# Performance work log

Measured on AMD Instinct MI355X. Metric: run time of the kernel, lower is better.

The kernel has to match this reference:

```python
import jax, jax.numpy as jnp
import numpy as np

N = 25000
E = 400000
HIDDEN = 512
NH = 8
DH = HIDDEN // NH


def setup_inputs() -> dict:
    key = jax.random.key(0)
    ks = jax.random.split(key, 10)
    s = 1.0 / np.sqrt(HIDDEN)
    return {
        "h": jax.random.normal(ks[0], (N, HIDDEN), dtype=jnp.float32),
        "Wq": jax.random.normal(ks[1], (HIDDEN, HIDDEN), dtype=jnp.float32) * s,
        "bq": jnp.zeros((HIDDEN,), dtype=jnp.float32),
        "Wk": jax.random.normal(ks[2], (HIDDEN, HIDDEN), dtype=jnp.float32) * s,
        "bk": jnp.zeros((HIDDEN,), dtype=jnp.float32),
        "Wo": jax.random.normal(ks[3], (HIDDEN, HIDDEN), dtype=jnp.float32) * s,
        "bo": jnp.zeros((HIDDEN,), dtype=jnp.float32),
        "rows": jax.random.randint(ks[4], (E,), 0, N, dtype=jnp.int32),
        "cols": jax.random.randint(ks[5], (E,), 0, N, dtype=jnp.int32),
    }


def reference(h, Wq, bq, Wk, bk, Wo, bo, rows, cols):
    # Projections; reshape (N, dh, nh) exactly as the source does.
    q = (h @ Wq + bq).reshape(N, DH, NH)
    k = (h @ Wk + bk).reshape(N, DH, NH)
    v = k  # source bug kept faithfully: v = linear_k(h)

    # SDDMM: per-edge, per-head dot product (no 1/sqrt(dh) scaling in source).
    scores = jnp.einsum("edh,edh->eh", q[rows], k[cols])  # [E, NH]

    # Row-wise (source-node) segment softmax per head.
    m = jax.ops.segment_max(scores, rows, num_segments=N)       # [N, NH]
    ex = jnp.exp(scores - m[rows])                              # [E, NH]
    denom = jax.ops.segment_sum(ex, rows, num_segments=N)      # [N, NH]
    attn = ex / denom[rows]                                     # [E, NH]

    # SpMM: out[i] = sum_{j in nbr(i)} attn[ij] * v[j]
    msgs = attn[:, None, :] * v[cols]                           # [E, DH, NH]
    out = jax.ops.segment_sum(msgs, rows, num_segments=N)      # [N, DH, NH]

    return out.reshape(N, HIDDEN) @ Wo + bo
```

## Files before the change

kernel.cpp:

```cpp
#include <hip/hip_runtime.h>
#include <math.h>

typedef unsigned short u16;
typedef unsigned int u32;
typedef __attribute__((ext_vector_type(8))) _Float16 half8;
typedef __attribute__((ext_vector_type(2))) _Float16 half2v;
typedef __attribute__((ext_vector_type(8))) u16 ushort8;
typedef __attribute__((ext_vector_type(4))) float f32x4;

__device__ __forceinline__ u16 f2h(float f) {
    union { u16 u; _Float16 h; } c; c.h = (_Float16)f; return c.u;
}

#if __has_builtin(__builtin_amdgcn_fdot2)
#define FDOT2(a, b, c) __builtin_amdgcn_fdot2((a), (b), (c), false)
#else
#define FDOT2(a, b, c) fmaf((float)(a)[0], (float)(b)[0], \
                        fmaf((float)(a)[1], (float)(b)[1], (c)))
#endif

__device__ __forceinline__ void gload16(void* lds, const void* g) {
    __builtin_amdgcn_global_load_lds(
        (const __attribute__((address_space(1))) u32*)g,
        (__attribute__((address_space(3))) u32*)lds,
        16, 0, 0);
}

template <int OUTMODE>
__device__ __forceinline__ void gemm_body(
    const u16* A, const u16* Bt, const float* bias, void* Cout, int Mout,
    int m0, int n0, u16* AsB, u16* BsB)
{
    const int tid  = threadIdx.x;
    const int wave = tid >> 6;
    const int lane = tid & 63;
    const int wr = (wave >> 1) * 64;
    const int wc = (wave & 1) * 64;

    f32x4 acc[4][4];
#pragma unroll
    for (int i = 0; i < 4; ++i)
#pragma unroll
        for (int j = 0; j < 4; ++j) acc[i][j] = (f32x4){0.f, 0.f, 0.f, 0.f};

    const int srow  = lane >> 2;
    const int scolG = ((lane & 3) ^ ((srow >> 1) & 3)) * 8;
    const size_t gOffA = (size_t)(m0 + wave * 32 + srow) * 512 + scolG;
    const size_t gOffB = (size_t)(n0 + wave * 32 + srow) * 512 + scolG;
    const int lOff = wave * 1024 + srow * 32 + (lane & 3) * 8;

    const int fR = ((lane & 15) >> 1) & 3;
    const int paOff = (wr + (lane & 15)) * 32 + ((lane >> 4) ^ fR) * 8;
    const int pbOff = (wc + (lane & 15)) * 32 + ((lane >> 4) ^ fR) * 8;

    auto STAGE = [&](int buf, int ko) {
        u16* sa = AsB + buf * 4096;
        u16* sb = BsB + buf * 4096;
        gload16(sa + lOff,       A  + gOffA + ko);
        gload16(sa + lOff + 512, A  + gOffA + ko + 16 * 512);
        gload16(sb + lOff,       Bt + gOffB + ko);
        gload16(sb + lOff + 512, Bt + gOffB + ko + 16 * 512);
    };
    auto COMPUTE = [&](int buf) {
        const u16* sa = AsB + buf * 4096;
        const u16* sb = BsB + buf * 4096;
        half8 af[4], bf[4];
#pragma unroll
        for (int i = 0; i < 4; ++i) af[i] = *(const half8*)(sa + paOff + i * 512);
#pragma unroll
        for (int j = 0; j < 4; ++j) bf[j] = *(const half8*)(sb + pbOff + j * 512);
#pragma unroll
        for (int i = 0; i < 4; ++i)
#pragma unroll
            for (int j = 0; j < 4; ++j)
                acc[i][j] = __builtin_amdgcn_mfma_f32_16x16x32_f16(
                    af[i], bf[j], acc[i][j], 0, 0, 0);
    };

    STAGE(0, 0);
    STAGE(1, 32);
#pragma unroll
    for (int kt = 0; kt < 16; ++kt) {
        if (kt < 15) asm volatile("s_waitcnt vmcnt(4)" ::: "memory");
        else         asm volatile("s_waitcnt vmcnt(0)" ::: "memory");
        __builtin_amdgcn_s_barrier();
        __builtin_amdgcn_sched_barrier(0);
        if (kt + 2 < 16) STAGE((kt + 2) % 3, (kt + 2) * 32);
        COMPUTE(kt % 3);
    }

    const int ccol  = n0 + wc + (lane & 15);
    const int crow0 = m0 + wr + (lane >> 4) * 4;
#pragma unroll
    for (int j = 0; j < 4; ++j) {
        const float b = bias[ccol + j * 16];
#pragma unroll
        for (int i = 0; i < 4; ++i) {
#pragma unroll
            for (int r = 0; r < 4; ++r) {
                int row = crow0 + i * 16 + r;
                if (row < Mout) {
                    float v = acc[i][j][r] + b;
                    size_t off = (size_t)row * 512 + ccol + j * 16;
                    if (OUTMODE == 0) ((float*)Cout)[off] = v;
                    else              ((u16*)Cout)[off] = f2h(v);
                }
            }
        }
    }
}

__global__ __launch_bounds__(256) void gemm_qk(
    const u16* __restrict__ hh, const u16* __restrict__ Wqt,
    const u16* __restrict__ Wkt, const float* __restrict__ bqp,
    const float* __restrict__ bkp, u16* __restrict__ Qh,
    u16* __restrict__ Kb, int nPad,
    const int* __restrict__ rows, const int* __restrict__ cols,
    int* __restrict__ cursor, int* __restrict__ colc, int E, int nGemm)
{
    __shared__ __align__(16) u16 AsB[3 * 4096], BsB[3 * 4096];
    const int bid = blockIdx.x;
    if (bid >= nGemm) {
        int i = (bid - nGemm) * 256 + threadIdx.x;
        if (i < E) {
            int pos = atomicAdd(&cursor[rows[i]], 1);
            colc[pos] = cols[i];
        }
        return;
    }
    const int m = (bid >> 6) * 8 + (bid & 7);
    const int s = (bid >> 3) & 7;
    if (m >= nPad / 128) return;
    const int z = s >> 2;
    const int n = s & 3;

    const u16* Bt = z ? Wkt : Wqt;
    const float* bias = z ? bkp : bqp;
    u16* out = z ? Kb : Qh;
    gemm_body<1>(hh, Bt, bias, out, nPad, m * 128, n * 128, AsB, BsB);
}

__global__ __launch_bounds__(256) void gemm_wo(
    const u16* __restrict__ A, const u16* __restrict__ Wot,
    const float* __restrict__ bo, float* __restrict__ C, int Mout, int nPad)
{
    const int bid = blockIdx.x;
    const int m = (bid >> 5) * 8 + (bid & 7);
    const int s = (bid >> 3) & 3;
    if (m >= nPad / 128) return;

    __shared__ __align__(16) u16 AsB[3 * 4096], BsB[3 * 4096];
    gemm_body<0>(A, Wot, bo, C, Mout, m * 128, s * 128, AsB, BsB);
}

__global__ __launch_bounds__(256) void prep(
    const float* __restrict__ h, u16* __restrict__ hh, int nN,
    const int* __restrict__ rows, int* __restrict__ deg, int E,
    const float* __restrict__ Wq, const float* __restrict__ Wk,
    const float* __restrict__ Wo, const float* __restrict__ bq,
    const float* __restrict__ bk,
    u16* __restrict__ Wqt, u16* __restrict__ Wkt, u16* __restrict__ Wot,
    float* __restrict__ bqp, float* __restrict__ bkp,
    int nbH, int nbE)
{
    __shared__ float T[64][65];
    const int tid = threadIdx.x;
    const int b = blockIdx.x;

    if (b < nbH) {
        int t = b * 256 + tid;
        size_t e = (size_t)t * 8;
        int row = (int)(e >> 9);
        ushort8 o;
        if (row < nN) {
            f32x4 a = *(const f32x4*)(h + e);
            f32x4 bb = *(const f32x4*)(h + e + 4);
            float x[8] = {a.x, a.y, a.z, a.w, bb.x, bb.y, bb.z, bb.w};
#pragma unroll
            for (int i = 0; i < 8; ++i) o[i] = f2h(x[i]);
        } else {
            o = (ushort8){0,0,0,0,0,0,0,0};
        }
        *(ushort8*)(hh + e) = o;
        return;
    }
    if (b < nbH + nbE) {
        int i = (b - nbH) * 256 + tid;
        if (i < E) atomicAdd(&deg[rows[i]], 1);
        return;
    }
    int rem = b - nbH - nbE;
    const int z = rem >> 6;
    const int X = (rem & 7) * 64;
    const int Y = ((rem >> 3) & 7) * 64;

    const int r4 = tid >> 4;
    const int c4 = (tid & 15) * 4;
    if (z < 2) {
        const float* W = z ? Wk : Wq;
#pragma unroll
        for (int rr = 0; rr < 64; rr += 16) {
            f32x4 v = *(const f32x4*)(W + (size_t)(X + rr + r4) * 512 + Y + c4);
            T[rr + r4][c4 + 0] = v.x; T[rr + r4][c4 + 1] = v.y;
            T[rr + r4][c4 + 2] = v.z; T[rr + r4][c4 + 3] = v.w;
        }
    } else {
#pragma unroll
        for (int rr = 0; rr < 64; rr += 16) {
            int p2 = (rr + r4) * 8 + (X >> 6);
            f32x4 v = *(const f32x4*)(Wo + (size_t)p2 * 512 + Y + c4);
            T[rr + r4][c4 + 0] = v.x; T[rr + r4][c4 + 1] = v.y;
            T[rr + r4][c4 + 2] = v.z; T[rr + r4][c4 + 3] = v.w;
        }
    }
    __syncthreads();

    const int cc = tid >> 2;
    const int ks = (tid & 3) * 16;
    const int pc = Y + cc;
    const int ro = (z < 2) ? ((pc & 7) * 64 + (pc >> 3)) : pc;
    ushort8 h0, h1;
#pragma unroll
    for (int t = 0; t < 8; ++t) {
        h0[t] = f2h(T[ks + t][cc]);
        h1[t] = f2h(T[ks + 8 + t][cc]);
    }
    size_t o = (size_t)ro * 512 + X + ks;
    if (z == 0) {
        *(ushort8*)(Wqt + o) = h0; *(ushort8*)(Wqt + o + 8) = h1;
    } else if (z == 1) {
        *(ushort8*)(Wkt + o) = h0; *(ushort8*)(Wkt + o + 8) = h1;
    } else {
        *(ushort8*)(Wot + o) = h0; *(ushort8*)(Wot + o + 8) = h1;
        if (rem == 128) {
            for (int bi = tid; bi < 512; bi += 256) {
                int pp = (bi & 63) * 8 + (bi >> 6);
                bqp[bi] = bq[pp];
                bkp[bi] = bk[pp];
            }
        }
    }
}

#define SCAN_CHUNK 2048

__global__ __launch_bounds__(256) void scan_partial(
    const int* __restrict__ deg, int* __restrict__ bsum, int n)
{
    int base = blockIdx.x * SCAN_CHUNK;
    int t = threadIdx.x;
    int s = 0;
    for (int i = t; i < SCAN_CHUNK; i += 256) {
        int g = base + i;
        s += (g < n) ? deg[g] : 0;
    }
#pragma unroll
    for (int off = 1; off < 64; off <<= 1) s += __shfl_xor(s, off, 64);
    __shared__ int ws[4];
    if ((t & 63) == 0) ws[t >> 6] = s;
    __syncthreads();
    if (t == 0) bsum[blockIdx.x] = ws[0] + ws[1] + ws[2] + ws[3];
}

__global__ __launch_bounds__(256) void scan_final(
    const int* __restrict__ deg, const int* __restrict__ bsum,
    int* __restrict__ rowptr, int* __restrict__ cursor, int n, int nb)
{
    int boff = 0, total = 0;
    for (int i = 0; i < nb; ++i) {
        int v = bsum[i];
        if (i < (int)blockIdx.x) boff += v;
        total += v;
    }
    int t = threadIdx.x;
    int base = blockIdx.x * SCAN_CHUNK + t * 8;
    int v[8];
    int s = 0;
#pragma unroll
    for (int i = 0; i < 8; ++i) {
        int g = base + i;
        v[i] = (g < n) ? deg[g] : 0;
        s += v[i];
    }
    int lane = t & 63, w = t >> 6;
    int inc = s;
#pragma unroll
    for (int off = 1; off < 64; off <<= 1) {
        int x = __shfl_up(inc, off, 64);
        if (lane >= off) inc += x;
    }
    __shared__ int wsum[4];
    if (lane == 63) wsum[w] = inc;
    __syncthreads();
    int excl = boff + inc - s;
    for (int i = 0; i < w; ++i) excl += wsum[i];
#pragma unroll
    for (int i = 0; i < 8; ++i) {
        int g = base + i;
        if (g < n) { rowptr[g] = excl; cursor[g] = excl; }
        excl += v[i];
    }
    if (blockIdx.x == 0 && t == 0) rowptr[n] = total;
}

__global__ __launch_bounds__(256) void node_agg(
    const u16* __restrict__ Qh, const u16* __restrict__ Kb,
    const int* __restrict__ rowptr, const int* __restrict__ colc,
    u16* __restrict__ aggb, int nN)
{
    int node = blockIdx.x * 4 + (threadIdx.x >> 6);
    int lane = threadIdx.x & 63;
    if (node >= nN) return;
    size_t base = (size_t)node * 512 + lane * 8;

    half8 qv = __builtin_nontemporal_load((const half8*)(Qh + base));
    half2v q2[4];
#pragma unroll
    for (int i = 0; i < 4; ++i) q2[i] = (half2v){qv[2 * i], qv[2 * i + 1]};

    int start = rowptr[node];
    int deg   = rowptr[node + 1] - start;
    const int* cp = colc + start;
    const size_t loff = (size_t)lane * 8;

    float m = -__builtin_inff();
    float den = 0.f;
    half2v acc2[4];
#pragma unroll
    for (int i = 0; i < 4; ++i) acc2[i] = (half2v){(_Float16)0.f, (_Float16)0.f};

    if (deg > 0) {
        const int dl = deg - 1;
        half8 k[8];
#pragma unroll
        for (int t = 0; t < 8; ++t) {
            int it = t < dl ? t : dl;
            k[t] = *(const half8*)(Kb + (size_t)cp[it] * 512 + loff);
        }
        for (int j = 0; j < deg; j += 8) {
            half8 nx[8];
#pragma unroll
            for (int t = 0; t < 8; ++t) {
                int it = j + 8 + t < dl ? j + 8 + t : dl;
                nx[t] = *(const half8*)(Kb + (size_t)cp[it] * 512 + loff);
            }

            float p[8];
#pragma unroll
            for (int t = 0; t < 8; ++t) {
                float s = 0.f;
#pragma unroll
                for (int i = 0; i < 4; ++i) {
                    half2v bb = (half2v){k[t][2 * i], k[t][2 * i + 1]};
                    s = FDOT2(q2[i], bb, s);
                }
                p[t] = s;
            }
#pragma unroll
            for (int off = 1; off < 8; off <<= 1) {
#pragma unroll
                for (int t = 0; t < 8; ++t) p[t] += __shfl_xor(p[t], off, 64);
            }

            float pm = p[0];
#pragma unroll
            for (int t = 1; t < 8; ++t) pm = fmaxf(pm, p[t]);
            if (__any(pm > m + 4.f)) {
                float mn = fmaxf(m, pm);
                float sc = __expf(m - mn);
                den *= sc;
                _Float16 sch = (_Float16)sc;
                half2v sc2 = {sch, sch};
#pragma unroll
                for (int i = 0; i < 4; ++i) acc2[i] *= sc2;
                m = mn;
            }
#pragma unroll
            for (int t = 0; t < 8; ++t) {
                float w = (j + t < deg) ? __expf(p[t] - m) : 0.f;
                den += w;
                _Float16 wh = (_Float16)w;
                half2v w2 = {wh, wh};
#pragma unroll
                for (int i = 0; i < 4; ++i) {
                    half2v bb = (half2v){k[t][2 * i], k[t][2 * i + 1]};
                    acc2[i] += w2 * bb;
                }
            }
#pragma unroll
            for (int t = 0; t < 8; ++t) k[t] = nx[t];
        }
    }

    float inv = (deg > 0) ? 1.f / den : 0.f;
    ushort8 o;
#pragma unroll
    for (int i = 0; i < 4; ++i) {
        o[2 * i]     = f2h((float)acc2[i][0] * inv);
        o[2 * i + 1] = f2h((float)acc2[i][1] * inv);
    }
    __builtin_nontemporal_store(o, (ushort8*)(aggb + base));
}

extern "C" void kernel_launch(void* const* d_in, const int* in_sizes, int n_in,
                              void* d_out, int out_size, void* d_ws, size_t ws_size,
                              hipStream_t stream)
{
    const float* h  = (const float*)d_in[0];
    const float* Wq = (const float*)d_in[1];
    const float* bq = (const float*)d_in[2];
    const float* Wk = (const float*)d_in[3];
    const float* bk = (const float*)d_in[4];
    const float* Wo = (const float*)d_in[5];
    const float* bo = (const float*)d_in[6];
    const int* rows = (const int*)d_in[7];
    const int* cols = (const int*)d_in[8];
    float* out = (float*)d_out;

    const int HID = 512;
    const int nN  = in_sizes[0] / HID;
    const int E   = in_sizes[7];
    const int nPad = (nN + 127) & ~127;
    const int nb = (nN + SCAN_CHUNK - 1) / SCAN_CHUNK;
    const int nbH = nPad * (HID / 8) / 256;
    const int nbE = (E + 255) / 256;
    const int nMt = nPad / 128;
    const int nGrp = (nMt + 7) / 8;
    const int nGemmQK = nGrp * 64;

    char* w = (char*)d_ws;
    u16* Kb  = (u16*)w;  w += (size_t)nPad * HID * 2;
    u16* hh  = (u16*)w;  w += (size_t)nPad * HID * 2;
    u16* Qh  = (u16*)w;  w += (size_t)nPad * HID * 2;
    u16* Wqt = (u16*)w;  w += 512 * 512 * 2;
    u16* Wkt = (u16*)w;  w += 512 * 512 * 2;
    u16* Wot = (u16*)w;  w += 512 * 512 * 2;
    float* bqp = (float*)w;  w += 512 * 4;
    float* bkp = (float*)w;  w += 512 * 4;
    int* rowptr = (int*)w;   w += (size_t)(nN + 1) * 4;
    int* cursor = (int*)w;   w += (size_t)nN * 4;
    int* deg    = (int*)w;   w += (size_t)nN * 4;
    int* bsum   = (int*)w;   w += 64 * 4;
    int* colc   = (int*)w;

    (void)hipMemsetAsync(deg, 0, (size_t)nN * sizeof(int), stream);

    prep<<<nbH + nbE + 192, 256, 0, stream>>>(
        h, hh, nN, rows, deg, E, Wq, Wk, Wo, bq, bk,
        Wqt, Wkt, Wot, bqp, bkp, nbH, nbE);

    scan_partial<<<nb, 256, 0, stream>>>(deg, bsum, nN);
    scan_final<<<nb, 256, 0, stream>>>(deg, bsum, rowptr, cursor, nN, nb);

    gemm_qk<<<nGemmQK + nbE, 256, 0, stream>>>(
        hh, Wqt, Wkt, bqp, bkp, Qh, Kb, nPad,
        rows, cols, cursor, colc, E, nGemmQK);

    node_agg<<<(nN + 3) / 4, 256, 0, stream>>>(Qh, Kb, rowptr, colc, hh, nN);

    gemm_wo<<<nGrp * 32, 256, 0, stream>>>(hh, Wot, bo, out, nN, nPad);
}
```

Baseline: 243.5 us.

## Switch GEMM to double-buffered LDS pipeline and merge scan kernels into one

```diff
diff --git a/kernel.cpp b/kernel.cpp
--- a/kernel.cpp
+++ b/kernel.cpp
@@ -29,7 +29,7 @@
 template <int OUTMODE>
 __device__ __forceinline__ void gemm_body(
     const u16* A, const u16* Bt, const float* bias, void* Cout, int Mout,
-    int m0, int n0, u16* AsB, u16* BsB)
+    int m0, int n0, u16* As0, u16* As1, u16* Bs0, u16* Bs1)
 {
     const int tid  = threadIdx.x;
     const int wave = tid >> 6;
@@ -53,17 +53,13 @@
     const int paOff = (wr + (lane & 15)) * 32 + ((lane >> 4) ^ fR) * 8;
     const int pbOff = (wc + (lane & 15)) * 32 + ((lane >> 4) ^ fR) * 8;
 
-    auto STAGE = [&](int buf, int ko) {
-        u16* sa = AsB + buf * 4096;
-        u16* sb = BsB + buf * 4096;
+    auto STAGE = [&](u16* sa, u16* sb, int ko) {
         gload16(sa + lOff,       A  + gOffA + ko);
         gload16(sa + lOff + 512, A  + gOffA + ko + 16 * 512);
         gload16(sb + lOff,       Bt + gOffB + ko);
         gload16(sb + lOff + 512, Bt + gOffB + ko + 16 * 512);
     };
-    auto COMPUTE = [&](int buf) {
-        const u16* sa = AsB + buf * 4096;
-        const u16* sb = BsB + buf * 4096;
+    auto COMPUTE = [&](const u16* sa, const u16* sb) {
         half8 af[4], bf[4];
 #pragma unroll
         for (int i = 0; i < 4; ++i) af[i] = *(const half8*)(sa + paOff + i * 512);
@@ -77,16 +73,16 @@
                     af[i], bf[j], acc[i][j], 0, 0, 0);
     };
 
-    STAGE(0, 0);
-    STAGE(1, 32);
-#pragma unroll
-    for (int kt = 0; kt < 16; ++kt) {
-        if (kt < 15) asm volatile("s_waitcnt vmcnt(4)" ::: "memory");
-        else         asm volatile("s_waitcnt vmcnt(0)" ::: "memory");
-        __builtin_amdgcn_s_barrier();
-        __builtin_amdgcn_sched_barrier(0);
-        if (kt + 2 < 16) STAGE((kt + 2) % 3, (kt + 2) * 32);
-        COMPUTE(kt % 3);
+    STAGE(As0, Bs0, 0);
+    __syncthreads();
+#pragma unroll
+    for (int kt = 0; kt < 16; kt += 2) {
+        STAGE(As1, Bs1, (kt + 1) * 32);
+        COMPUTE(As0, Bs0);
+        __syncthreads();
+        if (kt + 2 < 16) STAGE(As0, Bs0, (kt + 2) * 32);
+        COMPUTE(As1, Bs1);
+        __syncthreads();
     }
 
     const int ccol  = n0 + wc + (lane & 15);
@@ -118,7 +114,7 @@
     const int* __restrict__ rows, const int* __restrict__ cols,
     int* __restrict__ cursor, int* __restrict__ colc, int E, int nGemm)
 {
-    __shared__ __align__(16) u16 AsB[3 * 4096], BsB[3 * 4096];
+    __shared__ __align__(16) u16 As0[4096], As1[4096], Bs0[4096], Bs1[4096];
     const int bid = blockIdx.x;
     if (bid >= nGemm) {
         int i = (bid - nGemm) * 256 + threadIdx.x;
@@ -137,7 +133,8 @@
     const u16* Bt = z ? Wkt : Wqt;
     const float* bias = z ? bkp : bqp;
     u16* out = z ? Kb : Qh;
-    gemm_body<1>(hh, Bt, bias, out, nPad, m * 128, n * 128, AsB, BsB);
+    gemm_body<1>(hh, Bt, bias, out, nPad, m * 128, n * 128,
+                 As0, As1, Bs0, Bs1);
 }
 
 __global__ __launch_bounds__(256) void gemm_wo(
@@ -149,8 +146,9 @@
     const int s = (bid >> 3) & 3;
     if (m >= nPad / 128) return;
 
-    __shared__ __align__(16) u16 AsB[3 * 4096], BsB[3 * 4096];
-    gemm_body<0>(A, Wot, bo, C, Mout, m * 128, s * 128, AsB, BsB);
+    __shared__ __align__(16) u16 As0[4096], As1[4096], Bs0[4096], Bs1[4096];
+    gemm_body<0>(A, Wot, bo, C, Mout, m * 128, s * 128,
+                 As0, As1, Bs0, Bs1);
 }
 
 __global__ __launch_bounds__(256) void prep(
@@ -244,36 +242,24 @@
 
 #define SCAN_CHUNK 2048
 
-__global__ __launch_bounds__(256) void scan_partial(
-    const int* __restrict__ deg, int* __restrict__ bsum, int n)
-{
-    int base = blockIdx.x * SCAN_CHUNK;
-    int t = threadIdx.x;
-    int s = 0;
-    for (int i = t; i < SCAN_CHUNK; i += 256) {
-        int g = base + i;
-        s += (g < n) ? deg[g] : 0;
-    }
-#pragma unroll
-    for (int off = 1; off < 64; off <<= 1) s += __shfl_xor(s, off, 64);
-    __shared__ int ws[4];
-    if ((t & 63) == 0) ws[t >> 6] = s;
+__global__ __launch_bounds__(256) void scan_all(
+    const int* __restrict__ deg, int* __restrict__ rowptr,
+    int* __restrict__ cursor, int n, int nb)
+{
+    const int t = threadIdx.x;
+    const int b = blockIdx.x;
+    const int lane = t & 63, wv = t >> 6;
+    __shared__ int ws[4], wsum[4];
+
+    int pre = 0;
+    for (int i = t; i < b * SCAN_CHUNK; i += 256) pre += deg[i];
+#pragma unroll
+    for (int off = 1; off < 64; off <<= 1) pre += __shfl_xor(pre, off, 64);
+    if (lane == 0) ws[wv] = pre;
     __syncthreads();
-    if (t == 0) bsum[blockIdx.x] = ws[0] + ws[1] + ws[2] + ws[3];
-}
-
-__global__ __launch_bounds__(256) void scan_final(
-    const int* __restrict__ deg, const int* __restrict__ bsum,
-    int* __restrict__ rowptr, int* __restrict__ cursor, int n, int nb)
-{
-    int boff = 0, total = 0;
-    for (int i = 0; i < nb; ++i) {
-        int v = bsum[i];
-        if (i < (int)blockIdx.x) boff += v;
-        total += v;
-    }
-    int t = threadIdx.x;
-    int base = blockIdx.x * SCAN_CHUNK + t * 8;
+    const int boff = ws[0] + ws[1] + ws[2] + ws[3];
+
+    int base = b * SCAN_CHUNK + t * 8;
     int v[8];
     int s = 0;
 #pragma unroll
@@ -282,25 +268,24 @@
         v[i] = (g < n) ? deg[g] : 0;
         s += v[i];
     }
-    int lane = t & 63, w = t >> 6;
     int inc = s;
 #pragma unroll
     for (int off = 1; off < 64; off <<= 1) {
         int x = __shfl_up(inc, off, 64);
         if (lane >= off) inc += x;
     }
-    __shared__ int wsum[4];
-    if (lane == 63) wsum[w] = inc;
+    if (lane == 63) wsum[wv] = inc;
     __syncthreads();
     int excl = boff + inc - s;
-    for (int i = 0; i < w; ++i) excl += wsum[i];
+    for (int i = 0; i < wv; ++i) excl += wsum[i];
 #pragma unroll
     for (int i = 0; i < 8; ++i) {
         int g = base + i;
         if (g < n) { rowptr[g] = excl; cursor[g] = excl; }
         excl += v[i];
     }
-    if (blockIdx.x == 0 && t == 0) rowptr[n] = total;
+    if (b == nb - 1 && t == 0)
+        rowptr[n] = boff + wsum[0] + wsum[1] + wsum[2] + wsum[3];
 }
 
 __global__ __launch_bounds__(256) void node_agg(
@@ -449,8 +434,7 @@
         h, hh, nN, rows, deg, E, Wq, Wk, Wo, bq, bk,
         Wqt, Wkt, Wot, bqp, bkp, nbH, nbE);
 
-    scan_partial<<<nb, 256, 0, stream>>>(deg, bsum, nN);
-    scan_final<<<nb, 256, 0, stream>>>(deg, bsum, rowptr, cursor, nN, nb);
+    scan_all<<<nb, 256, 0, stream>>>(deg, rowptr, cursor, nN, nb);
 
     gemm_qk<<<nGemmQK + nbE, 256, 0, stream>>>(
         hh, Wqt, Wkt, bqp, bkp, Qh, Kb, nPad,
```

Result: faster. 226.2 us (-7.1%).
